# Performance work log

Hardware: AMD Instinct MI355X
Metric: run time of the kernel (lower is better)

The kernel has to match this reference:

```python
import jax, jax.numpy as jnp
import numpy as np

THETA_BASE = 10000.0

def rope(x, pos_offset=0):
    # x: (B, S, D), D even. Rotates interleaved (even, odd) dim pairs.
    B, S, D = x.shape
    pos = jnp.arange(pos_offset, pos_offset + S, dtype=jnp.float32)[:, None]  # (S,1)
    p = jnp.arange(D // 2, dtype=jnp.float32)  # p-1 in source, 0-indexed here
    theta = pos * (THETA_BASE ** (-2.0 * p / D))  # (S, D//2)
    sin_t, cos_t = jnp.sin(theta), jnp.cos(theta)
    x1, x2 = x[..., 0::2], x[..., 1::2]
    r1 = x1 * cos_t - x2 * sin_t
    r2 = x1 * sin_t + x2 * cos_t
    return jnp.stack((r1, r2), axis=-1).reshape(B, S, D)

def setup_inputs() -> dict:
    key = jax.random.key(0)
    k1, k2, k3, k4 = jax.random.split(key, 4)
    B, S, E, Dh = 4, 4096, 2048, 128
    return {
        "x": jax.random.normal(k1, (B, S, E), dtype=jnp.float32),
        "W_Q": jax.random.normal(k2, (E, Dh), dtype=jnp.float32) / np.sqrt(E),
        "W_K": jax.random.normal(k3, (E, Dh), dtype=jnp.float32) / np.sqrt(E),
        "W_V": jax.random.normal(k4, (E, Dh), dtype=jnp.float32) / np.sqrt(E),
    }

def reference(x, W_Q, W_K, W_V):
    d_h = W_Q.shape[1]
    past_len = 0  # kv_cache is None (prefill)
    Q = rope(x @ W_Q, pos_offset=past_len)  # NOTE: source ropes Q and V, not K
    K = x @ W_K
    V = rope(x @ W_V, pos_offset=past_len)
    scores = jnp.einsum('bqd,bkd->bqk', Q, K) / jnp.sqrt(jnp.float32(d_h))
    S_q, S_total = scores.shape[-2], scores.shape[-1]
    i = jnp.arange(S_q)[:, None] + past_len
    j = jnp.arange(S_total)[None, :]
    causal = j <= i  # (S_q, S_total) bool
    masked = jnp.where(causal[None, :, :], scores, jnp.float32(-jnp.inf))
    attn = jax.nn.softmax(masked, axis=-1)
    return jnp.einsum('bqk,bkd->bqd', attn, V)
```

## Files before the change

### kernel.cpp

```cpp
#include <hip/hip_runtime.h>
#include <hip/hip_bf16.h>
#include <stdint.h>

#define S_LEN 4096
#define E_DIM 2048
#define DH    128

typedef __bf16 bf16_t;
typedef bf16_t bf16x8 __attribute__((ext_vector_type(8)));
typedef float  f32x4  __attribute__((ext_vector_type(4)));

__device__ __forceinline__ unsigned short f2bf(float f) {
  union { float f; uint32_t u; } v; v.f = f;
  uint32_t u = v.u;
  uint32_t r = (u + 0x7fffu + ((u >> 16) & 1u)) >> 16;
  return (unsigned short)r;
}

__device__ __forceinline__ bf16x8 ld_bf16x8(const unsigned short* p) {
  return *(const bf16x8*)p;
}

__device__ __forceinline__ f32x4 mfma16(bf16x8 a, bf16x8 b, f32x4 c) {
  return __builtin_amdgcn_mfma_f32_16x16x32_bf16(a, b, c, 0, 0, 0);
}

__device__ __forceinline__ void gload16(const void* gsrc, void* ldst) {
  __builtin_amdgcn_global_load_lds(
      (const __attribute__((address_space(1))) uint32_t*)gsrc,
      (__attribute__((address_space(3))) uint32_t*)ldst, 16, 0, 0);
}

__global__ __launch_bounds__(256) void prep_kernel(
    const float* __restrict__ WQ, const float* __restrict__ WK,
    const float* __restrict__ WV,
    float2* __restrict__ trig, unsigned short* __restrict__ Wt)
{
  const int bx  = blockIdx.x;
  const int tid = threadIdx.x;
  if (bx < 1024) {
    const int idx = bx * 256 + tid;
    const int pos = idx >> 6, p = idx & 63;
    const float freq = powf(10000.0f, -(float)p / 64.0f);
    float sv, cv;
    sincosf((float)pos * freq, &sv, &cv);
    trig[idx] = make_float2(cv, sv);
    return;
  }
  __shared__ float lds[64][65];
  const int t   = bx - 1024;
  const int z   = t >> 6;
  const int rem = t & 63;
  const int k0  = (rem >> 1) * 64;
  const int n0  = (rem & 1) * 64;
  const float* W = (z == 0) ? WQ : ((z == 1) ? WK : WV);
  #pragma unroll
  for (int pass = 0; pass < 4; pass++) {
    const int r  = pass * 16 + (tid >> 4);
    const int c4 = (tid & 15) * 4;
    float4 v = *(const float4*)(W + (size_t)(k0 + r) * 128 + n0 + c4);
    lds[c4 + 0][r] = v.x; lds[c4 + 1][r] = v.y;
    lds[c4 + 2][r] = v.z; lds[c4 + 3][r] = v.w;
  }
  __syncthreads();
  #pragma unroll
  for (int pass = 0; pass < 4; pass++) {
    const int n  = pass * 16 + (tid >> 4);
    const int k4 = (tid & 15) * 4;
    ushort4 pk;
    pk.x = f2bf(lds[n][k4 + 0]); pk.y = f2bf(lds[n][k4 + 1]);
    pk.z = f2bf(lds[n][k4 + 2]); pk.w = f2bf(lds[n][k4 + 3]);
    *(ushort4*)(Wt + (size_t)(z * 128 + n0 + n) * E_DIM + k0 + k4) = pk;
  }
}

__global__ __launch_bounds__(256, 4) void proj_kernel(
    const float* __restrict__ x, const unsigned short* __restrict__ Wt,
    const float2* __restrict__ trig,
    unsigned short* __restrict__ Qb, unsigned short* __restrict__ Kb,
    unsigned short* __restrict__ Vt)
{
  __shared__ __align__(16) uint8_t Abuf[2][64 * 128];
  __shared__ __align__(16) uint8_t Bbuf[2][96 * 128];

  const int tid  = threadIdx.x;
  const int lane = tid & 63, w2 = tid >> 6;
  const int wr = w2 & 1, wc = w2 >> 1;
  const int col = lane & 15, kg = lane >> 4;

  const int m0 = blockIdx.x * 64;
  const int p  = blockIdx.y;

  f32x4 acc[2][3];
  #pragma unroll
  for (int i = 0; i < 2; i++)
    #pragma unroll
    for (int j = 0; j < 3; j++) acc[i][j] = (f32x4){0.f, 0.f, 0.f, 0.f};

  const int a_r = lane >> 4;
  const int a_c = (lane & 15) * 4;
  const int b_r  = lane >> 3;
  const int b_cb = (lane & 7) * 16;

  float4 a_reg[4];

  #define ALOAD(K0)                                                           \
    do {                                                                      \
      _Pragma("unroll")                                                       \
      for (int j = 0; j < 4; j++) {                                           \
        const int row = w2 * 16 + j * 4 + a_r;                                \
        a_reg[j] = *(const float4*)(x + (size_t)(m0 + row) * E_DIM + (K0) + a_c);\
      }                                                                       \
    } while (0)

  #define BSTAGE(K0, BUF)                                                     \
    do {                                                                      \
      _Pragma("unroll")                                                       \
      for (int c = 0; c < 3; c++) {                                           \
        const int seg = w2 * 3 + c;                                           \
        const int row = seg * 8 + b_r;                                        \
        const int src = b_cb ^ ((row & 7) << 4);                              \
        gload16((const char*)Wt + ((size_t)(p * 96 + row) * E_DIM + (K0)) * 2 + src,\
                &Bbuf[BUF][seg * 1024]);                                      \
      }                                                                       \
    } while (0)

  #define AWRITE(BUF)                                                         \
    do {                                                                      \
      _Pragma("unroll")                                                       \
      for (int j = 0; j < 4; j++) {                                           \
        const int row = w2 * 16 + j * 4 + a_r;                                \
        ushort4 h;                                                            \
        h.x = f2bf(a_reg[j].x); h.y = f2bf(a_reg[j].y);                       \
        h.z = f2bf(a_reg[j].z); h.w = f2bf(a_reg[j].w);                       \
        const int dst = (a_c * 2) ^ ((row & 7) << 4);                         \
        *(ushort4*)(&Abuf[BUF][row * 128 + dst]) = h;                         \
      }                                                                       \
    } while (0)

  ALOAD(0);
  BSTAGE(0, 0);
  AWRITE(0);
  __syncthreads();

  int cur = 0;
  for (int t = 0; t < 32; t++) {
    if (t < 31) {
      ALOAD((t + 1) * 64);
      BSTAGE((t + 1) * 64, cur ^ 1);
    }

    __builtin_amdgcn_s_setprio(1);
    #pragma unroll
    for (int kk = 0; kk < 2; kk++) {
      bf16x8 af[2];
      #pragma unroll
      for (int i = 0; i < 2; i++) {
        const int row = wr * 32 + i * 16 + col;
        af[i] = *(const bf16x8*)(&Abuf[cur][row * 128 +
                 ((kk * 64 + kg * 16) ^ ((row & 7) << 4))]);
      }
      #pragma unroll
      for (int ns = 0; ns < 3; ns++) {
        const int n = wc * 48 + ns * 16 + col;
        bf16x8 bf = *(const bf16x8*)(&Bbuf[cur][n * 128 +
                    ((kk * 64 + kg * 16) ^ ((n & 7) << 4))]);
        #pragma unroll
        for (int i = 0; i < 2; i++)
          acc[i][ns] = mfma16(af[i], bf, acc[i][ns]);
      }
    }
    __builtin_amdgcn_s_setprio(0);

    if (t < 31) AWRITE(cur ^ 1);
    __syncthreads();
    cur ^= 1;
  }
  #undef ALOAD
  #undef BSTAGE
  #undef AWRITE

  #pragma unroll
  for (int i = 0; i < 2; i++) {
    const int mbase = m0 + wr * 32 + i * 16 + kg * 4;
    const int spos  = mbase & 4095;
    const int bb    = mbase >> 12;
    #pragma unroll
    for (int ns = 0; ns < 3; ns++) {
      const int n = p * 96 + wc * 48 + ns * 16 + col;
      const int z = n >> 7, d = n & 127;
      f32x4 v = acc[i][ns];
      if (z == 1) {
        #pragma unroll
        for (int r = 0; r < 4; r++)
          Kb[(size_t)(mbase + r) * DH + d] = f2bf(v[r]);
      } else {
        const float sgn  = (d & 1) ? 1.0f : -1.0f;
        const int   pidx = d >> 1;
        float ov[4];
        #pragma unroll
        for (int r = 0; r < 4; r++) {
          float  pv = __shfl_xor(v[r], 1, 64);
          float2 cs = trig[(spos + r) * 64 + pidx];
          ov[r] = v[r] * cs.x + sgn * pv * cs.y;
        }
        if (z == 0) {
          #pragma unroll
          for (int r = 0; r < 4; r++)
            Qb[(size_t)(mbase + r) * DH + d] =
                f2bf(ov[r] * 0.08838834764831845f);
        } else {
          ushort4 pk;
          pk.x = f2bf(ov[0]); pk.y = f2bf(ov[1]);
          pk.z = f2bf(ov[2]); pk.w = f2bf(ov[3]);
          *(ushort4*)(Vt + ((size_t)(bb * DH + d)) * S_LEN + spos) = pk;
        }
      }
    }
  }
}

__global__ __launch_bounds__(256, 2) void flash_kernel(
    const unsigned short* __restrict__ Qb, const unsigned short* __restrict__ Kb,
    const unsigned short* __restrict__ Vt, float* __restrict__ out)
{
  __shared__ __align__(16) unsigned short Ktile[128 * 128];
  __shared__ __align__(16) unsigned short Vtile[128 * 128];
  __shared__ __align__(16) unsigned short Plds[4][16][72];

  const int bid  = blockIdx.x;
  const int half = bid >> 8, rb = bid & 255;
  const int qi   = half ? (127 - (rb >> 1)) : (rb >> 1);
  const int b    = (rb & 1) | (half << 1);
  const int q0   = qi * 32;

  const int tid = threadIdx.x;
  const int lane = tid & 63, w = tid >> 6;
  const int h   = w & 1;
  const int kvh = w >> 1;
  const int col = lane & 15, kg = lane >> 4;

  bf16x8 qf[4];
  {
    const unsigned short* qrow =
        Qb + (size_t)(b * S_LEN + q0 + h * 16 + col) * DH;
    #pragma unroll
    for (int kk = 0; kk < 4; kk++)
      qf[kk] = ld_bf16x8(qrow + kk * 32 + kg * 8);
  }

  f32x4 o[8];
  #pragma unroll
  for (int i = 0; i < 8; i++) o[i] = (f32x4){0.f, 0.f, 0.f, 0.f};
  float mrow[4] = {-1e30f, -1e30f, -1e30f, -1e30f};
  float lrow[4] = {0.f, 0.f, 0.f, 0.f};

  const char* Kbase = (const char*)(Kb + (size_t)b * S_LEN * DH);
  const char* Vbase = (const char*)(Vt + (size_t)b * DH * S_LEN);

  const int r_off = lane >> 4, colb = (lane & 15) * 16;

  for (int kv0 = 0; kv0 < q0 + 32; kv0 += 128) {
    #pragma unroll
    for (int c = 0; c < 8; c++) {
      const int row = w * 32 + c * 4 + r_off;
      const int src = colb ^ ((row & 7) << 4);
      gload16(Kbase + (size_t)(kv0 + row) * 256 + src,
              (char*)Ktile + w * 8192 + c * 1024);
    }
    #pragma unroll
    for (int c = 0; c < 8; c++) {
      const int d   = w * 32 + c * 4 + r_off;
      const int src = colb ^ ((d & 7) << 4);
      gload16(Vbase + (size_t)d * 8192 + (size_t)kv0 * 2 + src,
              (char*)Vtile + w * 8192 + c * 1024);
    }
    __syncthreads();

    f32x4 st[4];
    __builtin_amdgcn_s_setprio(1);
    #pragma unroll
    for (int kb = 0; kb < 4; kb++) {
      f32x4 sacc = (f32x4){0.f, 0.f, 0.f, 0.f};
      const int krow = kvh * 64 + kb * 16 + col;
      #pragma unroll
      for (int kk = 0; kk < 4; kk++) {
        bf16x8 kf = *(const bf16x8*)((const char*)Ktile + krow * 256 +
                                     ((kk * 64 + kg * 16) ^ ((krow & 7) << 4)));
        sacc = mfma16(qf[kk], kf, sacc);
      }
      st[kb] = sacc;
    }
    __builtin_amdgcn_s_setprio(0);

    if (kv0 + 127 > q0) {
      #pragma unroll
      for (int kb = 0; kb < 4; kb++) {
        const int key = kv0 + kvh * 64 + kb * 16 + col;
        #pragma unroll
        for (int r = 0; r < 4; r++) {
          const int q = q0 + h * 16 + kg * 4 + r;
          if (key > q) st[kb][r] = -1e30f;
        }
      }
    }

    float scale[4];
    #pragma unroll
    for (int r = 0; r < 4; r++) {
      float mx = fmaxf(fmaxf(st[0][r], st[1][r]), fmaxf(st[2][r], st[3][r]));
      #pragma unroll
      for (int off = 1; off < 16; off <<= 1)
        mx = fmaxf(mx, __shfl_xor(mx, off, 64));
      const float mnew = fmaxf(mrow[r], mx);
      scale[r] = __expf(mrow[r] - mnew);
      mrow[r] = mnew;
      float psum = 0.f;
      #pragma unroll
      for (int kb = 0; kb < 4; kb++) {
        float pexp = __expf(st[kb][r] - mnew);
        st[kb][r] = pexp;
        psum += pexp;
      }
      lrow[r] = lrow[r] * scale[r] + psum;
    }
    #pragma unroll
    for (int nt = 0; nt < 8; nt++)
      #pragma unroll
      for (int r = 0; r < 4; r++)
        o[nt][r] *= scale[r];

    #pragma unroll
    for (int kb = 0; kb < 4; kb++)
      #pragma unroll
      for (int r = 0; r < 4; r++)
        Plds[w][kg * 4 + r][kb * 16 + col] = f2bf(st[kb][r]);

    __builtin_amdgcn_s_setprio(1);
    #pragma unroll
    for (int kc = 0; kc < 2; kc++) {
      bf16x8 pa = ld_bf16x8(&Plds[w][col][kc * 32 + kg * 8]);
      #pragma unroll
      for (int nt = 0; nt < 8; nt++) {
        const int vrow = nt * 16 + col;
        bf16x8 vf = *(const bf16x8*)((const char*)Vtile + vrow * 256 +
            ((kvh * 128 + kc * 64 + kg * 16) ^ ((vrow & 7) << 4)));
        o[nt] = mfma16(pa, vf, o[nt]);
      }
    }
    __builtin_amdgcn_s_setprio(0);
    __syncthreads();
  }

  float lfull[4];
  #pragma unroll
  for (int r = 0; r < 4; r++) {
    float l = lrow[r];
    #pragma unroll
    for (int off = 1; off < 16; off <<= 1)
      l += __shfl_xor(l, off, 64);
    lfull[r] = l;
  }

  float* Olds = (float*)Ktile;
  float* Ml   = (float*)Vtile;
  #pragma unroll
  for (int nt = 0; nt < 8; nt++)
    #pragma unroll
    for (int r = 0; r < 4; r++)
      Olds[(w * 16 + kg * 4 + r) * 128 + nt * 16 + col] = o[nt][r];
  if (col == 0) {
    #pragma unroll
    for (int r = 0; r < 4; r++) {
      Ml[w * 16 + kg * 4 + r]      = mrow[r];
      Ml[64 + w * 16 + kg * 4 + r] = lfull[r];
    }
  }
  __syncthreads();
  if (w < 2) {
    #pragma unroll
    for (int r = 0; r < 4; r++) {
      const int row = kg * 4 + r;
      const float m1 = Ml[w * 16 + row],        l1 = Ml[64 + w * 16 + row];
      const float m2 = Ml[(w + 2) * 16 + row],  l2 = Ml[64 + (w + 2) * 16 + row];
      const float mf = fmaxf(m1, m2);
      const float w1 = __expf(m1 - mf), wgt2 = __expf(m2 - mf);
      const float inv = 1.0f / (l1 * w1 + l2 * wgt2);
      float* orow = out + (size_t)(b * S_LEN + q0 + w * 16 + row) * DH;
      #pragma unroll
      for (int nt = 0; nt < 8; nt++) {
        const float v1 = Olds[(w * 16 + row) * 128 + nt * 16 + col];
        const float v2 = Olds[((w + 2) * 16 + row) * 128 + nt * 16 + col];
        orow[nt * 16 + col] = (v1 * w1 + v2 * wgt2) * inv;
      }
    }
  }
}

extern "C" void kernel_launch(void* const* d_in, const int* in_sizes, int n_in,
                              void* d_out, int out_size, void* d_ws, size_t ws_size,
                              hipStream_t stream) {
  const float* x  = (const float*)d_in[0];
  const float* WQ = (const float*)d_in[1];
  const float* WK = (const float*)d_in[2];
  const float* WV = (const float*)d_in[3];
  float* out = (float*)d_out;

  char* ws = (char*)d_ws;
  float2*         trig = (float2*)(ws);
  unsigned short* Wt   = (unsigned short*)(ws + (2u << 20));
  unsigned short* Qb   = (unsigned short*)(ws + (4u << 20));
  unsigned short* Kb   = (unsigned short*)(ws + (8u << 20));
  unsigned short* Vt   = (unsigned short*)(ws + (12u << 20));

  hipLaunchKernelGGL(prep_kernel, dim3(1216), dim3(256), 0, stream,
                     WQ, WK, WV, trig, Wt);
  hipLaunchKernelGGL(proj_kernel, dim3(256, 4), dim3(256), 0, stream,
                     x, Wt, trig, Qb, Kb, Vt);
  hipLaunchKernelGGL(flash_kernel, dim3(512), dim3(256), 0, stream,
                     Qb, Kb, Vt, out);
}
```

Baseline: 138.7 us.

## Load projection GEMM operands directly from global into registers, dropping LDS staging

The QKV projection kernel no longer stages x and W tiles through double-buffered shared memory with swizzling and barriers. Each lane now loads its MFMA fragments straight from global memory into registers, double-buffered across two half-steps of K, and converts x to bf16 in registers. This removes LDS traffic and __syncthreads, but each wave re-fetches data that was previously shared across waves, which raises global and L2 traffic and leaves loads less coalesced.

```diff
diff --git a/kernel.cpp b/kernel.cpp
--- a/kernel.cpp
+++ b/kernel.cpp
@@ -80,9 +80,6 @@
     unsigned short* __restrict__ Qb, unsigned short* __restrict__ Kb,
     unsigned short* __restrict__ Vt)
 {
-  __shared__ __align__(16) uint8_t Abuf[2][64 * 128];
-  __shared__ __align__(16) uint8_t Bbuf[2][96 * 128];
-
   const int tid  = threadIdx.x;
   const int lane = tid & 63, w2 = tid >> 6;
   const int wr = w2 & 1, wc = w2 >> 1;
@@ -91,94 +88,62 @@
   const int m0 = blockIdx.x * 64;
   const int p  = blockIdx.y;
 
+  const float* xr0 = x + (size_t)(m0 + wr * 32 + col) * E_DIM + kg * 8;
+  const float* xr1 = xr0 + 16 * E_DIM;
+  const unsigned short* wb0 =
+      Wt + (size_t)(p * 96 + wc * 48 + col) * E_DIM + kg * 8;
+  const unsigned short* wb1 = wb0 + 16 * E_DIM;
+  const unsigned short* wb2 = wb0 + 32 * E_DIM;
+
   f32x4 acc[2][3];
   #pragma unroll
   for (int i = 0; i < 2; i++)
     #pragma unroll
     for (int j = 0; j < 3; j++) acc[i][j] = (f32x4){0.f, 0.f, 0.f, 0.f};
 
-  const int a_r = lane >> 4;
-  const int a_c = (lane & 15) * 4;
-  const int b_r  = lane >> 3;
-  const int b_cb = (lane & 7) * 16;
-
-  float4 a_reg[4];
-
-  #define ALOAD(K0)                                                           \
-    do {                                                                      \
-      _Pragma("unroll")                                                       \
-      for (int j = 0; j < 4; j++) {                                           \
-        const int row = w2 * 16 + j * 4 + a_r;                                \
-        a_reg[j] = *(const float4*)(x + (size_t)(m0 + row) * E_DIM + (K0) + a_c);\
-      }                                                                       \
-    } while (0)
-
-  #define BSTAGE(K0, BUF)                                                     \
-    do {                                                                      \
-      _Pragma("unroll")                                                       \
-      for (int c = 0; c < 3; c++) {                                           \
-        const int seg = w2 * 3 + c;                                           \
-        const int row = seg * 8 + b_r;                                        \
-        const int src = b_cb ^ ((row & 7) << 4);                              \
-        gload16((const char*)Wt + ((size_t)(p * 96 + row) * E_DIM + (K0)) * 2 + src,\
-                &Bbuf[BUF][seg * 1024]);                                      \
-      }                                                                       \
-    } while (0)
-
-  #define AWRITE(BUF)                                                         \
-    do {                                                                      \
-      _Pragma("unroll")                                                       \
-      for (int j = 0; j < 4; j++) {                                           \
-        const int row = w2 * 16 + j * 4 + a_r;                                \
-        ushort4 h;                                                            \
-        h.x = f2bf(a_reg[j].x); h.y = f2bf(a_reg[j].y);                       \
-        h.z = f2bf(a_reg[j].z); h.w = f2bf(a_reg[j].w);                       \
-        const int dst = (a_c * 2) ^ ((row & 7) << 4);                         \
-        *(ushort4*)(&Abuf[BUF][row * 128 + dst]) = h;                         \
-      }                                                                       \
-    } while (0)
-
-  ALOAD(0);
-  BSTAGE(0, 0);
-  AWRITE(0);
-  __syncthreads();
-
-  int cur = 0;
+  float4 A0[4], A1[4];
+  bf16x8 B0[3], B1[3];
+
+  auto LOADA = [&](float4* A, int k0) {
+    A[0] = *(const float4*)(xr0 + k0);
+    A[1] = *(const float4*)(xr0 + k0 + 4);
+    A[2] = *(const float4*)(xr1 + k0);
+    A[3] = *(const float4*)(xr1 + k0 + 4);
+  };
+  auto LOADB = [&](bf16x8* B, int k0) {
+    B[0] = ld_bf16x8(wb0 + k0);
+    B[1] = ld_bf16x8(wb1 + k0);
+    B[2] = ld_bf16x8(wb2 + k0);
+  };
+  auto COMP = [&](const float4* A, const bf16x8* B) {
+    bf16x8 af[2];
+    #pragma unroll
+    for (int i = 0; i < 2; i++) {
+      af[i][0] = (bf16_t)A[i * 2].x;     af[i][1] = (bf16_t)A[i * 2].y;
+      af[i][2] = (bf16_t)A[i * 2].z;     af[i][3] = (bf16_t)A[i * 2].w;
+      af[i][4] = (bf16_t)A[i * 2 + 1].x; af[i][5] = (bf16_t)A[i * 2 + 1].y;
+      af[i][6] = (bf16_t)A[i * 2 + 1].z; af[i][7] = (bf16_t)A[i * 2 + 1].w;
+    }
+    #pragma unroll
+    for (int ns = 0; ns < 3; ns++)
+      #pragma unroll
+      for (int i = 0; i < 2; i++)
+        acc[i][ns] = mfma16(af[i], B[ns], acc[i][ns]);
+  };
+
+  LOADA(A0, 0);
+  LOADB(B0, 0);
   for (int t = 0; t < 32; t++) {
+    const int kbase = t * 64;
+    LOADA(A1, kbase + 32);
+    LOADB(B1, kbase + 32);
+    COMP(A0, B0);
     if (t < 31) {
-      ALOAD((t + 1) * 64);
-      BSTAGE((t + 1) * 64, cur ^ 1);
-    }
-
-    __builtin_amdgcn_s_setprio(1);
-    #pragma unroll
-    for (int kk = 0; kk < 2; kk++) {
-      bf16x8 af[2];
-      #pragma unroll
-      for (int i = 0; i < 2; i++) {
-        const int row = wr * 32 + i * 16 + col;
-        af[i] = *(const bf16x8*)(&Abuf[cur][row * 128 +
-                 ((kk * 64 + kg * 16) ^ ((row & 7) << 4))]);
-      }
-      #pragma unroll
-      for (int ns = 0; ns < 3; ns++) {
-        const int n = wc * 48 + ns * 16 + col;
-        bf16x8 bf = *(const bf16x8*)(&Bbuf[cur][n * 128 +
-                    ((kk * 64 + kg * 16) ^ ((n & 7) << 4))]);
-        #pragma unroll
-        for (int i = 0; i < 2; i++)
-          acc[i][ns] = mfma16(af[i], bf, acc[i][ns]);
-      }
-    }
-    __builtin_amdgcn_s_setprio(0);
-
-    if (t < 31) AWRITE(cur ^ 1);
-    __syncthreads();
-    cur ^= 1;
-  }
-  #undef ALOAD
-  #undef BSTAGE
-  #undef AWRITE
+      LOADA(A0, kbase + 64);
+      LOADB(B0, kbase + 64);
+    }
+    COMP(A1, B1);
+  }
 
   #pragma unroll
   for (int i = 0; i < 2; i++) {
```

After: 281.9 us. 103% more time.

## Deepen QKV projection pipeline with double-buffered A registers and explicit waitcnts

Applied to the files above, without the earlier changes.

Restructures the QKV projection GEMM main loop so the fp32 x tiles are loaded two K-steps ahead into two alternating register sets. The loop is unrolled by two, and explicit vmcnt/lgkmcnt waits, sched_barriers and raw s_barrier replace __syncthreads. The aim is to hide global-load latency for the A operand behind more MFMA work and stop the compiler from conservatively draining all memory counters. In exchange it uses more registers and hand-counted waitcnt values, which break if the number of loads changes. The s_setprio hints are dropped.

```diff
diff --git a/kernel.cpp b/kernel.cpp
--- a/kernel.cpp
+++ b/kernel.cpp
@@ -102,14 +102,14 @@
   const int b_r  = lane >> 3;
   const int b_cb = (lane & 7) * 16;
 
-  float4 a_reg[4];
-
-  #define ALOAD(K0)                                                           \
+  float4 R0[4], R1[4];
+
+  #define ALOAD(R, K0)                                                        \
     do {                                                                      \
       _Pragma("unroll")                                                       \
       for (int j = 0; j < 4; j++) {                                           \
         const int row = w2 * 16 + j * 4 + a_r;                                \
-        a_reg[j] = *(const float4*)(x + (size_t)(m0 + row) * E_DIM + (K0) + a_c);\
+        R[j] = *(const float4*)(x + (size_t)(m0 + row) * E_DIM + (K0) + a_c); \
       }                                                                       \
     } while (0)
 
@@ -125,60 +125,90 @@
       }                                                                       \
     } while (0)
 
-  #define AWRITE(BUF)                                                         \
+  #define AWRITE(R, BUF)                                                      \
     do {                                                                      \
       _Pragma("unroll")                                                       \
       for (int j = 0; j < 4; j++) {                                           \
         const int row = w2 * 16 + j * 4 + a_r;                                \
         ushort4 h;                                                            \
-        h.x = f2bf(a_reg[j].x); h.y = f2bf(a_reg[j].y);                       \
-        h.z = f2bf(a_reg[j].z); h.w = f2bf(a_reg[j].w);                       \
+        h.x = f2bf(R[j].x); h.y = f2bf(R[j].y);                               \
+        h.z = f2bf(R[j].z); h.w = f2bf(R[j].w);                               \
         const int dst = (a_c * 2) ^ ((row & 7) << 4);                         \
         *(ushort4*)(&Abuf[BUF][row * 128 + dst]) = h;                         \
       }                                                                       \
     } while (0)
 
-  ALOAD(0);
+  #define COMP(BUF)                                                           \
+    do {                                                                      \
+      _Pragma("unroll")                                                       \
+      for (int kk = 0; kk < 2; kk++) {                                        \
+        bf16x8 af[2];                                                         \
+        _Pragma("unroll")                                                     \
+        for (int i = 0; i < 2; i++) {                                         \
+          const int row = wr * 32 + i * 16 + col;                             \
+          af[i] = *(const bf16x8*)(&Abuf[BUF][row * 128 +                     \
+                   ((kk * 64 + kg * 16) ^ ((row & 7) << 4))]);                \
+        }                                                                     \
+        _Pragma("unroll")                                                     \
+        for (int ns = 0; ns < 3; ns++) {                                      \
+          const int n = wc * 48 + ns * 16 + col;                              \
+          bf16x8 bf = *(const bf16x8*)(&Bbuf[BUF][n * 128 +                   \
+                      ((kk * 64 + kg * 16) ^ ((n & 7) << 4))]);               \
+          _Pragma("unroll")                                                   \
+          for (int i = 0; i < 2; i++)                                         \
+            acc[i][ns] = mfma16(af[i], bf, acc[i][ns]);                       \
+        }                                                                     \
+      }                                                                       \
+    } while (0)
+
   BSTAGE(0, 0);
-  AWRITE(0);
-  __syncthreads();
-
-  int cur = 0;
-  for (int t = 0; t < 32; t++) {
-    if (t < 31) {
-      ALOAD((t + 1) * 64);
-      BSTAGE((t + 1) * 64, cur ^ 1);
-    }
-
-    __builtin_amdgcn_s_setprio(1);
-    #pragma unroll
-    for (int kk = 0; kk < 2; kk++) {
-      bf16x8 af[2];
-      #pragma unroll
-      for (int i = 0; i < 2; i++) {
-        const int row = wr * 32 + i * 16 + col;
-        af[i] = *(const bf16x8*)(&Abuf[cur][row * 128 +
-                 ((kk * 64 + kg * 16) ^ ((row & 7) << 4))]);
-      }
-      #pragma unroll
-      for (int ns = 0; ns < 3; ns++) {
-        const int n = wc * 48 + ns * 16 + col;
-        bf16x8 bf = *(const bf16x8*)(&Bbuf[cur][n * 128 +
-                    ((kk * 64 + kg * 16) ^ ((n & 7) << 4))]);
-        #pragma unroll
-        for (int i = 0; i < 2; i++)
-          acc[i][ns] = mfma16(af[i], bf, acc[i][ns]);
-      }
-    }
-    __builtin_amdgcn_s_setprio(0);
-
-    if (t < 31) AWRITE(cur ^ 1);
-    __syncthreads();
-    cur ^= 1;
-  }
+  __builtin_amdgcn_sched_barrier(0);
+  ALOAD(R0, 0);
+  ALOAD(R1, 64);
+  __builtin_amdgcn_sched_barrier(0);
+  AWRITE(R0, 0);
+  asm volatile("s_waitcnt lgkmcnt(0)" ::: "memory");
+  __builtin_amdgcn_sched_barrier(0);
+  __builtin_amdgcn_s_barrier();
+
+  #define BODY(I, RLD, RWR)                                                   \
+    BSTAGE(((I) + 1) * 64, ((I) + 1) & 1);                                    \
+    __builtin_amdgcn_sched_barrier(0);                                        \
+    ALOAD(RLD, ((I) + 2) * 64);                                               \
+    __builtin_amdgcn_sched_barrier(0);                                        \
+    asm volatile("s_waitcnt vmcnt(11)" ::: "memory");                         \
+    __builtin_amdgcn_sched_barrier(0);                                        \
+    COMP((I) & 1);                                                            \
+    AWRITE(RWR, ((I) + 1) & 1);                                               \
+    asm volatile("s_waitcnt lgkmcnt(0)" ::: "memory");                        \
+    __builtin_amdgcn_sched_barrier(0);                                        \
+    __builtin_amdgcn_s_barrier();
+
+  for (int ii = 0; ii < 15; ii++) {
+    const int i0 = 2 * ii;
+    BODY(i0, R0, R1)
+    BODY(i0 + 1, R1, R0)
+  }
+
+  BSTAGE(31 * 64, 1);
+  __builtin_amdgcn_sched_barrier(0);
+  asm volatile("s_waitcnt vmcnt(7)" ::: "memory");
+  __builtin_amdgcn_sched_barrier(0);
+  COMP(0);
+  AWRITE(R1, 1);
+  asm volatile("s_waitcnt lgkmcnt(0)" ::: "memory");
+  __builtin_amdgcn_sched_barrier(0);
+  __builtin_amdgcn_s_barrier();
+
+  asm volatile("s_waitcnt vmcnt(0)" ::: "memory");
+  __builtin_amdgcn_sched_barrier(0);
+  COMP(1);
+
+  #undef BODY
   #undef ALOAD
   #undef BSTAGE
   #undef AWRITE
+  #undef COMP
 
   #pragma unroll
   for (int i = 0; i < 2; i++) {
```

Result: slower. 147.8 us (+6.6%).
